# Optimization experiments

Hardware: AMD Instinct MI355X
Metric: run time of the kernel (lower is better)

The kernel has to match this reference:

```python
import jax, jax.numpy as jnp
import numpy as np

N_NODES = 100000
N_EDGES = 1600000
C_IN = 128
C_OUT = 128


def setup_inputs() -> dict:
    key = jax.random.key(0)
    k1, k2, k3, k4, k5 = jax.random.split(key, 5)
    x = jax.random.normal(k1, (N_NODES, C_IN), dtype=jnp.float32)
    W = jax.random.normal(k2, (2 * C_IN, C_OUT), dtype=jnp.float32) * (1.0 / np.sqrt(2 * C_IN))
    b = jax.random.normal(k3, (C_OUT,), dtype=jnp.float32) * 0.01
    src = jax.random.randint(k4, (N_EDGES,), 0, N_NODES, dtype=jnp.int64 if jax.config.jax_enable_x64 else jnp.int32)
    dst = jax.random.randint(k5, (N_EDGES,), 0, N_NODES, dtype=jnp.int64 if jax.config.jax_enable_x64 else jnp.int32)
    return {"x": x, "W": W, "b": b, "src": src, "dst": dst}


def reference(x, W, b, src, dst):
    # Max-Relative graph conv: per-edge relative feature, max-aggregated per dst node.
    diff = x[dst] - x[src]                                  # [E, C]  (edge messages)
    max_diff = jax.ops.segment_max(diff, dst, num_segments=x.shape[0])  # [N, C]
    # Nodes with no incoming edges: segment_max yields -inf; zero them out.
    max_diff = jnp.where(jnp.isneginf(max_diff), jnp.zeros_like(max_diff), max_diff)
    h = jnp.concatenate([x, max_diff], axis=1)              # [N, 2C]
    return jax.nn.relu(h @ W + b)                           # Linear(2C->C_out) + ReLU
```

## Files before the change

### kernel.cpp

```cpp
#include <hip/hip_runtime.h>
#include <math.h>

#define NN 100000
#define NE 1600000
#define C 128

#define TS 4096
#define NT ((NE + TS - 1) / TS)
#define BUK ((NN + 511) >> 9)
#define NSC (BUK * NT)
#define NBS ((NSC + 2047) / 2048)
#define PREP_BLKS (NN * C / 8 / 256)
#define CONVW_BLKS (2 * C * C / 256)

typedef __attribute__((ext_vector_type(8))) short   bf16x8;
typedef __attribute__((ext_vector_type(4))) float   f32x4;
typedef unsigned short ushort_t;
typedef unsigned int   uint_t;

__device__ inline ushort_t f2bf(float f) {
    union { float f; uint_t u; } a; a.f = f;
    uint_t r = a.u + 0x7fff + ((a.u >> 16) & 1);
    return (ushort_t)(r >> 16);
}

__global__ __launch_bounds__(256) void k_setup(
        const float* __restrict__ x, ushort_t* __restrict__ xh,
        const float* __restrict__ W, ushort_t* __restrict__ Wt,
        const int* __restrict__ dst, int* __restrict__ tileHistT) {
    __shared__ int h[BUK];
    const int t  = threadIdx.x;
    const int bb = blockIdx.x;
    if (bb < PREP_BLKS) {
        int i = bb * 256 + t;
        int node = i >> 4;
        int c0   = (i & 15) * 8;
        const float4* xp = (const float4*)(x + (long)i * 8);
        float4 v0 = xp[0], v1 = xp[1];
        ushort_t o[8] = { f2bf(v0.x), f2bf(v0.y), f2bf(v0.z), f2bf(v0.w),
                          f2bf(v1.x), f2bf(v1.y), f2bf(v1.z), f2bf(v1.w) };
        *(bf16x8*)(xh + (long)node * 256 + c0) = *(bf16x8*)o;
    } else if (bb < PREP_BLKS + CONVW_BLKS) {
        int i = (bb - PREP_BLKS) * 256 + t;
        int k = i >> 7, n = i & 127;
        Wt[n * 256 + k] = f2bf(W[i]);
    } else {
        const int tile = bb - PREP_BLKS - CONVW_BLKS;
        for (int i = t; i < BUK; i += 256) h[i] = 0;
        __syncthreads();
        const int base = tile * TS;
        for (int i = t; i < TS; i += 256) {
            int e = base + i;
            if (e < NE) atomicAdd(&h[dst[e] >> 9], 1);
        }
        __syncthreads();
        for (int i = t; i < BUK; i += 256) tileHistT[i * NT + tile] = h[i];
    }
}

__global__ __launch_bounds__(256) void scan_partial(const int* __restrict__ in,
                                                    int* __restrict__ out,
                                                    int* __restrict__ blocksums,
                                                    int n) {
    __shared__ int ts[256];
    const int t = threadIdx.x;
    const int base = blockIdx.x * 2048 + t * 8;
    int c[8];
    int s = 0;
    #pragma unroll
    for (int j = 0; j < 8; ++j) {
        int i = base + j;
        c[j] = (i < n) ? in[i] : 0;
        s += c[j];
    }
    ts[t] = s;
    __syncthreads();
    for (int off = 1; off < 256; off <<= 1) {
        int add = (t >= off) ? ts[t - off] : 0;
        __syncthreads();
        ts[t] += add;
        __syncthreads();
    }
    int run = (t == 0) ? 0 : ts[t - 1];
    #pragma unroll
    for (int j = 0; j < 8; ++j) {
        int i = base + j;
        if (i < n) out[i] = run;
        run += c[j];
    }
    if (t == 255) blocksums[blockIdx.x] = ts[255];
}

__global__ __launch_bounds__(64) void scan_blocksums(const int* __restrict__ blocksums,
                                                     int* __restrict__ blockbase, int nb) {
    int lane = threadIdx.x;
    int v = (lane < nb) ? blocksums[lane] : 0;
    int incl = v;
    #pragma unroll
    for (int off = 1; off < 64; off <<= 1) {
        int nbr = __shfl_up(incl, off, 64);
        if (lane >= off) incl += nbr;
    }
    if (lane < nb) blockbase[lane] = incl - v;
}

__global__ __launch_bounds__(256) void p3_scatter(const int* __restrict__ dst,
                                                  const int* __restrict__ src,
                                                  const int* __restrict__ tileScan,
                                                  const int* __restrict__ blockbase,
                                                  uint_t* __restrict__ coarse) {
    __shared__ int cur[BUK];
    const int t = threadIdx.x, tile = blockIdx.x;
    for (int i = t; i < BUK; i += 256) {
        int idx = i * NT + tile;
        cur[i] = tileScan[idx] + blockbase[idx >> 11];
    }
    __syncthreads();
    const int base = tile * TS;
    for (int i = t; i < TS; i += 256) {
        int e = base + i;
        if (e < NE) {
            int d = dst[e];
            int p = atomicAdd(&cur[d >> 9], 1);
            coarse[p] = ((uint_t)(d & 511) << 17) | (uint_t)src[e];
        }
    }
}

__global__ __launch_bounds__(256) void p4_build(const uint_t* __restrict__ coarse,
                                                const int* __restrict__ tileScan,
                                                const int* __restrict__ blockbase,
                                                int* __restrict__ offs,
                                                int* __restrict__ ssrc) {
    __shared__ int cnt[512];
    __shared__ int ts[256];
    const int b = blockIdx.x, t = threadIdx.x;
    const int n0 = b << 9;
    const int i0 = b * NT;
    const int bs = tileScan[i0] + blockbase[i0 >> 11];
    int be;
    if (b == BUK - 1) be = NE;
    else { int i1 = (b + 1) * NT; be = tileScan[i1] + blockbase[i1 >> 11]; }
    cnt[t] = 0; cnt[t + 256] = 0;
    __syncthreads();
    for (int i = bs + t; i < be; i += 256)
        atomicAdd(&cnt[(int)(coarse[i] >> 17)], 1);
    __syncthreads();
    int c0 = cnt[2 * t], c1 = cnt[2 * t + 1];
    ts[t] = c0 + c1;
    __syncthreads();
    for (int off = 1; off < 256; off <<= 1) {
        int add = (t >= off) ? ts[t - off] : 0;
        __syncthreads();
        ts[t] += add;
        __syncthreads();
    }
    int ex = (t == 0) ? 0 : ts[t - 1];
    int o0 = bs + ex, o1 = o0 + c0;
    cnt[2 * t] = o0; cnt[2 * t + 1] = o1;
    if (n0 + 2 * t < NN)     offs[n0 + 2 * t]     = o0;
    if (n0 + 2 * t + 1 < NN) offs[n0 + 2 * t + 1] = o1;
    if (b == BUK - 1 && t == 0) offs[NN] = NE;
    __syncthreads();
    for (int i = bs + t; i < be; i += 256) {
        uint_t pk = coarse[i];
        int p = atomicAdd(&cnt[(int)(pk >> 17)], 1);
        ssrc[p] = (int)(pk & 0x1FFFF);
    }
}

#define ACCQ(u)  { m[0] = fminf(m[0], __uint_as_float((u).x << 16));          \
                   m[1] = fminf(m[1], __uint_as_float((u).x & 0xffff0000u));  \
                   m[2] = fminf(m[2], __uint_as_float((u).y << 16));          \
                   m[3] = fminf(m[3], __uint_as_float((u).y & 0xffff0000u));  \
                   m[4] = fminf(m[4], __uint_as_float((u).z << 16));          \
                   m[5] = fminf(m[5], __uint_as_float((u).z & 0xffff0000u));  \
                   m[6] = fminf(m[6], __uint_as_float((u).w << 16));          \
                   m[7] = fminf(m[7], __uint_as_float((u).w & 0xffff0000u)); }

__global__ __launch_bounds__(256) void node_min_v2(
        const int* __restrict__ offs, const int* __restrict__ ssrc,
        ushort_t* __restrict__ xh) {
    const int wid  = (blockIdx.x * 256 + threadIdx.x) >> 6;
    const int lane = threadIdx.x & 63;
    if (wid >= NN) return;
    const int g = lane >> 4;
    const int s = lane & 15;
    const int beg = offs[wid], end = offs[wid + 1];
    const char* xb = (const char*)xh;
    float m[8];
    #pragma unroll
    for (int j = 0; j < 8; ++j) m[j] = INFINITY;
    int i = beg;
    for (; i + 8 <= end; i += 8) {
        int e0 = ssrc[i + g];
        int e1 = ssrc[i + 4 + g];
        uint4 a = *(const uint4*)(xb + (long)e0 * 512 + s * 16);
        uint4 bq = *(const uint4*)(xb + (long)e1 * 512 + s * 16);
        ACCQ(a);
        ACCQ(bq);
    }
    for (; i < end; i += 4) {
        int e = i + g;
        int idx = ssrc[(e < end) ? e : (end - 1)];
        uint4 a = *(const uint4*)(xb + (long)idx * 512 + s * 16);
        if (e < end) ACCQ(a);
    }
    #pragma unroll
    for (int j = 0; j < 8; ++j) {
        m[j] = fminf(m[j], __shfl_xor(m[j], 16, 64));
        m[j] = fminf(m[j], __shfl_xor(m[j], 32, 64));
    }
    if (g == 0) {
        uint4 xd = *(const uint4*)(xb + (long)wid * 512 + s * 16);
        uint_t xu[4] = { xd.x, xd.y, xd.z, xd.w };
        bool has = end > beg;
        uint4 o;
        uint_t* op = (uint_t*)&o;
        #pragma unroll
        for (int j = 0; j < 4; ++j) {
            float lo = has ? (__uint_as_float(xu[j] << 16)         - m[2 * j])     : 0.0f;
            float hi = has ? (__uint_as_float(xu[j] & 0xffff0000u) - m[2 * j + 1]) : 0.0f;
            op[j] = (uint_t)f2bf(lo) | ((uint_t)f2bf(hi) << 16);
        }
        *(uint4*)((char*)xh + (long)wid * 512 + 256 + s * 16) = o;
    }
}

__global__ __launch_bounds__(256) void gemm_mfma(
        const ushort_t* __restrict__ xh, const ushort_t* __restrict__ Wt,
        const float* __restrict__ b, float* __restrict__ out) {
    const int w  = threadIdx.x >> 6;
    const int l  = threadIdx.x & 63;
    const int m0 = blockIdx.x * 64 + w * 16;
    int arow = m0 + (l & 15);
    if (arow >= NN) arow = NN - 1;
    const int kb = (l >> 4) * 8;

    f32x4 acc[8];
    #pragma unroll
    for (int n = 0; n < 8; ++n) acc[n] = (f32x4){0.f, 0.f, 0.f, 0.f};

    const ushort_t* ap    = xh + (long)arow * 256 + kb;
    const ushort_t* wbase = Wt + (l & 15) * 256 + kb;

    #pragma unroll
    for (int k0 = 0; k0 < 256; k0 += 32) {
        bf16x8 a = *(const bf16x8*)(ap + k0);
        #pragma unroll
        for (int n = 0; n < 8; ++n) {
            bf16x8 bb = *(const bf16x8*)(wbase + n * 16 * 256 + k0);
            acc[n] = __builtin_amdgcn_mfma_f32_16x16x32_bf16(a, bb, acc[n], 0, 0, 0);
        }
    }

    const int colb  = l & 15;
    const int rbase = m0 + ((l >> 4) << 2);
    #pragma unroll
    for (int n = 0; n < 8; ++n) {
        int col = n * 16 + colb;
        float bv = b[col];
        #pragma unroll
        for (int j = 0; j < 4; ++j) {
            int r = rbase + j;
            if (r < NN) out[(long)r * 128 + col] = fmaxf(acc[n][j] + bv, 0.0f);
        }
    }
}

__global__ void init_neginf(float* __restrict__ p, int n) {
    int i = blockIdx.x * blockDim.x + threadIdx.x;
    if (i < n) p[i] = -INFINITY;
}

__device__ inline void amaxf(float* a, float v, float cur) {
    if (cur >= v) return;
    if (v >= 0.0f) atomicMax((int*)a, __float_as_int(v));
    else           atomicMin((unsigned int*)a, __float_as_uint(v));
}

__global__ __launch_bounds__(256) void edge_max(
        const float* __restrict__ x, const int* __restrict__ src,
        const int* __restrict__ dst, float* __restrict__ maxdiff) {
    long tid = (long)blockIdx.x * blockDim.x + threadIdx.x;
    int e = (int)(tid >> 5);
    if (e >= NE) return;
    int lane = (int)(tid & 31);
    int s = src[e], d = dst[e];
    int c0 = lane * 4;
    const float4 xd = *(const float4*)(x + (long)d * C + c0);
    const float4 xs = *(const float4*)(x + (long)s * C + c0);
    float4 df;
    df.x = xd.x - xs.x; df.y = xd.y - xs.y;
    df.z = xd.z - xs.z; df.w = xd.w - xs.w;
    float* o = maxdiff + (long)d * C + c0;
    float4 cur = *(const float4*)o;
    amaxf(o + 0, df.x, cur.x);
    amaxf(o + 1, df.y, cur.y);
    amaxf(o + 2, df.z, cur.z);
    amaxf(o + 3, df.w, cur.w);
}

#define TN 32
__global__ __launch_bounds__(256) void gemm_relu(
        const float* __restrict__ x, const float* __restrict__ W,
        const float* __restrict__ b, float* __restrict__ out) {
    __shared__ float h[TN][2 * C];
    const int nb = blockIdx.x * TN;
    const int t  = threadIdx.x;
    for (int i = t; i < TN * 2 * C / 4; i += 256) {
        int idx  = i * 4;
        int node = idx / (2 * C);
        int ci   = idx % (2 * C);
        float4 v;
        if (ci < C) {
            v = *(const float4*)(x + (long)(nb + node) * C + ci);
        } else {
            v = *(const float4*)(out + (long)(nb + node) * C + (ci - C));
            if (v.x == -INFINITY) v.x = 0.0f;
            if (v.y == -INFINITY) v.y = 0.0f;
            if (v.z == -INFINITY) v.z = 0.0f;
            if (v.w == -INFINITY) v.w = 0.0f;
        }
        *(float4*)&h[node][ci] = v;
    }
    __syncthreads();
    const int co = (t & 31) * 4;
    const int n0 = (t >> 5) * 4;
    float acc[4][4];
    #pragma unroll
    for (int i = 0; i < 4; ++i)
        #pragma unroll
        for (int j = 0; j < 4; ++j) acc[i][j] = 0.0f;
    for (int ci = 0; ci < 2 * C; ++ci) {
        float4 w = *(const float4*)(W + (long)ci * C + co);
        #pragma unroll
        for (int i = 0; i < 4; ++i) {
            float hv = h[n0 + i][ci];
            acc[i][0] = fmaf(hv, w.x, acc[i][0]);
            acc[i][1] = fmaf(hv, w.y, acc[i][1]);
            acc[i][2] = fmaf(hv, w.z, acc[i][2]);
            acc[i][3] = fmaf(hv, w.w, acc[i][3]);
        }
    }
    float4 bias = *(const float4*)(b + co);
    #pragma unroll
    for (int i = 0; i < 4; ++i) {
        float4 r;
        r.x = fmaxf(acc[i][0] + bias.x, 0.0f);
        r.y = fmaxf(acc[i][1] + bias.y, 0.0f);
        r.z = fmaxf(acc[i][2] + bias.z, 0.0f);
        r.w = fmaxf(acc[i][3] + bias.w, 0.0f);
        *(float4*)(out + (long)(nb + n0 + i) * C + co) = r;
    }
}

extern "C" void kernel_launch(void* const* d_in, const int* in_sizes, int n_in,
                              void* d_out, int out_size, void* d_ws, size_t ws_size,
                              hipStream_t stream) {
    const float* x   = (const float*)d_in[0];
    const float* W   = (const float*)d_in[1];
    const float* b   = (const float*)d_in[2];
    const int*   src = (const int*)d_in[3];
    const int*   dst = (const int*)d_in[4];
    float* out = (float*)d_out;

    size_t ints_head = (size_t)128 + NSC + (NN + 1) + NE;
    size_t head_b    = ((ints_head * 4) + 255) & ~(size_t)255;
    size_t xh_b      = (size_t)NN * 256 * 2;
    size_t wt_b      = (size_t)2 * C * C * 2;
    size_t need      = head_b + xh_b + wt_b;

    if (ws_size >= need) {
        int* blocksums = (int*)d_ws;
        int* blockbase = blocksums + 64;
        int* tileScan  = blockbase + 64;
        int* offs      = tileScan + NSC;
        int* ssrc      = offs + NN + 1;
        ushort_t* xh   = (ushort_t*)((char*)d_ws + head_b);
        ushort_t* Wt   = (ushort_t*)((char*)d_ws + head_b + xh_b);
        int*    tileHistT = ssrc;
        uint_t* coarse    = (uint_t*)d_out;

        k_setup<<<PREP_BLKS + CONVW_BLKS + NT, 256, 0, stream>>>(x, xh, W, Wt, dst, tileHistT);
        scan_partial<<<NBS, 256, 0, stream>>>(tileHistT, tileScan, blocksums, NSC);
        scan_blocksums<<<1, 64, 0, stream>>>(blocksums, blockbase, NBS);
        p3_scatter<<<NT, 256, 0, stream>>>(dst, src, tileScan, blockbase, coarse);
        p4_build<<<BUK, 256, 0, stream>>>(coarse, tileScan, blockbase, offs, ssrc);
        node_min_v2<<<NN / 4, 256, 0, stream>>>(offs, ssrc, xh);
        gemm_mfma<<<(NN + 63) / 64, 256, 0, stream>>>(xh, Wt, b, out);
    } else {
        int n = NN * C;
        init_neginf<<<(n + 255) / 256, 256, 0, stream>>>(out, n);
        long threads = (long)NE * 32;
        edge_max<<<(int)((threads + 255) / 256), 256, 0, stream>>>(x, src, dst, out);
        gemm_relu<<<(NN + TN - 1) / TN, 256, 0, stream>>>(x, W, b, out);
    }
}
```

Baseline: 294.4 us.

## Restructure MFMA GEMM so each wave keeps a weight slice in registers

The GEMM's work split changes. Before, each wave handled 16 rows across all 128 output columns and reloaded weight fragments from global memory for every row tile. Now each wave owns 32 output columns and holds that weight slice in registers, then loops over four 16-row tiles that share the same A rows across the waves of the block. This cuts repeated weight loads, but it raises register pressure and means each A row is loaded by all four waves, relying on cache hits.

```diff
diff --git a/kernel.cpp b/kernel.cpp
--- a/kernel.cpp
+++ b/kernel.cpp
@@ -12,6 +12,7 @@
 #define NBS ((NSC + 2047) / 2048)
 #define PREP_BLKS (NN * C / 8 / 256)
 #define CONVW_BLKS (2 * C * C / 256)
+#define GM 64
 
 typedef __attribute__((ext_vector_type(8))) short   bf16x8;
 typedef __attribute__((ext_vector_type(4))) float   f32x4;
@@ -230,40 +231,52 @@
 __global__ __launch_bounds__(256) void gemm_mfma(
         const ushort_t* __restrict__ xh, const ushort_t* __restrict__ Wt,
         const float* __restrict__ b, float* __restrict__ out) {
-    const int w  = threadIdx.x >> 6;
-    const int l  = threadIdx.x & 63;
-    const int m0 = blockIdx.x * 64 + w * 16;
-    int arow = m0 + (l & 15);
-    if (arow >= NN) arow = NN - 1;
-    const int kb = (l >> 4) * 8;
-
-    f32x4 acc[8];
-    #pragma unroll
-    for (int n = 0; n < 8; ++n) acc[n] = (f32x4){0.f, 0.f, 0.f, 0.f};
-
-    const ushort_t* ap    = xh + (long)arow * 256 + kb;
-    const ushort_t* wbase = Wt + (l & 15) * 256 + kb;
-
-    #pragma unroll
-    for (int k0 = 0; k0 < 256; k0 += 32) {
-        bf16x8 a = *(const bf16x8*)(ap + k0);
-        #pragma unroll
-        for (int n = 0; n < 8; ++n) {
-            bf16x8 bb = *(const bf16x8*)(wbase + n * 16 * 256 + k0);
-            acc[n] = __builtin_amdgcn_mfma_f32_16x16x32_bf16(a, bb, acc[n], 0, 0, 0);
-        }
-    }
-
-    const int colb  = l & 15;
-    const int rbase = m0 + ((l >> 4) << 2);
-    #pragma unroll
-    for (int n = 0; n < 8; ++n) {
-        int col = n * 16 + colb;
-        float bv = b[col];
+    const int w    = threadIdx.x >> 6;
+    const int l    = threadIdx.x & 63;
+    const int wcol = w * 32;
+    const int lr   = l & 15;
+    const int kb   = (l >> 4) * 8;
+
+    bf16x8 bb[2][8];
+    float  bv[2];
+    #pragma unroll
+    for (int n = 0; n < 2; ++n) {
+        int col = wcol + n * 16 + lr;
+        bv[n] = b[col];
+        const ushort_t* wp = Wt + (long)col * 256 + kb;
+        #pragma unroll
+        for (int k0 = 0; k0 < 8; ++k0)
+            bb[n][k0] = *(const bf16x8*)(wp + k0 * 32);
+    }
+
+    const int mb0 = blockIdx.x * GM;
+    #pragma unroll
+    for (int mt = 0; mt < GM / 16; ++mt) {
+        int mbase = mb0 + mt * 16;
+        int arow = mbase + lr;
+        if (arow >= NN) arow = NN - 1;
+        const ushort_t* ap = xh + (long)arow * 256 + kb;
+        bf16x8 a[8];
+        #pragma unroll
+        for (int k0 = 0; k0 < 8; ++k0) a[k0] = *(const bf16x8*)(ap + k0 * 32);
+
+        f32x4 acc0 = (f32x4){0.f, 0.f, 0.f, 0.f};
+        f32x4 acc1 = (f32x4){0.f, 0.f, 0.f, 0.f};
+        #pragma unroll
+        for (int k0 = 0; k0 < 8; ++k0) {
+            acc0 = __builtin_amdgcn_mfma_f32_16x16x32_bf16(a[k0], bb[0][k0], acc0, 0, 0, 0);
+            acc1 = __builtin_amdgcn_mfma_f32_16x16x32_bf16(a[k0], bb[1][k0], acc1, 0, 0, 0);
+        }
+
+        int rbase = mbase + ((l >> 4) << 2);
+        int col0 = wcol + lr;
         #pragma unroll
         for (int j = 0; j < 4; ++j) {
             int r = rbase + j;
-            if (r < NN) out[(long)r * 128 + col] = fmaxf(acc[n][j] + bv, 0.0f);
+            if (r < NN) {
+                out[(long)r * 128 + col0]      = fmaxf(acc0[j] + bv[0], 0.0f);
+                out[(long)r * 128 + col0 + 16] = fmaxf(acc1[j] + bv[1], 0.0f);
+            }
         }
     }
 }
@@ -388,7 +401,7 @@
         p3_scatter<<<NT, 256, 0, stream>>>(dst, src, tileScan, blockbase, coarse);
         p4_build<<<BUK, 256, 0, stream>>>(coarse, tileScan, blockbase, offs, ssrc);
         node_min_v2<<<NN / 4, 256, 0, stream>>>(offs, ssrc, xh);
-        gemm_mfma<<<(NN + 63) / 64, 256, 0, stream>>>(xh, Wt, b, out);
+        gemm_mfma<<<(NN + GM - 1) / GM, 256, 0, stream>>>(xh, Wt, b, out);
     } else {
         int n = NN * C;
         init_neginf<<<(n + 255) / 256, 256, 0, stream>>>(out, n);
```

Result: faster. 269.4 us (-8.5%).
